# Performance work log

Hardware: AMD Instinct MI355X
Metric: run time of the kernel (lower is better)

The kernel has to match this reference:

```python
import jax, jax.numpy as jnp
import numpy as np

D_MODEL = 1024
N_HEADS = 16
HEAD_DIM = D_MODEL // N_HEADS
BATCH = 2
SEQ = 2048


def setup_inputs() -> dict:
    key = jax.random.key(0)
    ks = jax.random.split(key, 9)
    s = 1.0 / np.sqrt(D_MODEL)
    inp = {
        "x": jax.random.normal(ks[0], (BATCH, SEQ, D_MODEL), dtype=jnp.float32),
        "Wq": jax.random.uniform(ks[1], (D_MODEL, D_MODEL), jnp.float32, -s, s),
        "bq": jax.random.uniform(ks[2], (D_MODEL,), jnp.float32, -s, s),
        "Wk": jax.random.uniform(ks[3], (D_MODEL, D_MODEL), jnp.float32, -s, s),
        "bk": jax.random.uniform(ks[4], (D_MODEL,), jnp.float32, -s, s),
        "Wv": jax.random.uniform(ks[5], (D_MODEL, D_MODEL), jnp.float32, -s, s),
        "bv": jax.random.uniform(ks[6], (D_MODEL,), jnp.float32, -s, s),
        "Wo": jax.random.uniform(ks[7], (D_MODEL, D_MODEL), jnp.float32, -s, s),
        "bo": jax.random.uniform(ks[8], (D_MODEL,), jnp.float32, -s, s),
    }
    return inp


def reference(x, Wq, bq, Wk, bk, Wv, bv, Wo, bo):
    B, S, _ = x.shape
    # projections -> [B, H, S, Dh]
    def proj(W, b):
        y = jnp.einsum('bsd,df->bsf', x, W) + b
        return y.reshape(B, S, N_HEADS, HEAD_DIM).transpose(0, 2, 1, 3)
    q = proj(Wq, bq)
    k = proj(Wk, bk)
    v = proj(Wv, bv)
    scores = jnp.einsum('bhqd,bhkd->bhqk', q, k) / jnp.sqrt(jnp.float32(HEAD_DIM))
    mask = jnp.tril(jnp.ones((S, S), dtype=bool))  # [S, S] causal mask
    scores = jnp.where(mask, scores, -jnp.inf)
    weights = jax.nn.softmax(scores, axis=-1)
    h = jnp.einsum('bhqk,bhkd->bhqd', weights, v)
    h = h.transpose(0, 2, 1, 3).reshape(B, S, N_HEADS * HEAD_DIM)
    return jnp.einsum('bsd,df->bsf', h, Wo) + bo
```

## Files before the change

kernel.cpp:

```cpp
#include <hip/hip_runtime.h>
#include <hip/hip_bf16.h>
#include <cmath>

#define D_MODEL 1024
#define NHEADS 16
#define HDIM 64
#define BATCH 2
#define SEQ 2048
#define MROWS (BATCH*SEQ)
#define KDIM 1024

typedef unsigned short ushort_t;
typedef unsigned int uint32;
typedef __attribute__((ext_vector_type(8))) short short8;
typedef __attribute__((ext_vector_type(4))) float floatx4;

#define QSCALE 0.1803368801111204f
#define EXP2F(x) __builtin_amdgcn_exp2f(x)

__device__ __forceinline__ ushort_t f2bf(float x) {
    union { float f; uint32 u; } v; v.f = x;
    uint32 r = v.u + 0x7FFFu + ((v.u >> 16) & 1u);
    return (ushort_t)(r >> 16);
}

__device__ __forceinline__ uint32 pkbf(float a, float b) {
    union { __hip_bfloat162 h2; uint32 u; } v;
    v.h2 = __float22bfloat162_rn(make_float2(a, b));
    return v.u;
}

__device__ __forceinline__ void glds16(const void* g, void* l) {
    __builtin_amdgcn_global_load_lds(
        (const __attribute__((address_space(1))) void*)g,
        (__attribute__((address_space(3))) void*)l, 16, 0, 0);
}

__global__ __launch_bounds__(256)
void cvt_all(const float* __restrict__ x, const float* __restrict__ W0,
             const float* __restrict__ W1, const float* __restrict__ W2,
             const float* __restrict__ W3, ushort_t* __restrict__ xb,
             ushort_t* __restrict__ WtQKV, ushort_t* __restrict__ WtO)
{
    const int z = blockIdx.z;
    if (z == 4) {
        size_t idx = ((size_t)blockIdx.y * 32 + blockIdx.x) * 256 + threadIdx.x;
        #pragma unroll
        for (int l = 0; l < 4; ++l) {
            size_t i = ((size_t)l * 262144 + idx) * 4;
            float4 v = *(const float4*)(x + i);
            uint2 o;
            o.x = pkbf(v.x, v.y);
            o.y = pkbf(v.z, v.w);
            *(uint2*)(xb + i) = o;
        }
        return;
    }
    __shared__ float tl[32][33];
    const float* W = (z == 0) ? W0 : (z == 1) ? W1 : (z == 2) ? W2 : W3;
    ushort_t* out = (z < 3) ? (WtQKV + (size_t)z * D_MODEL * KDIM) : WtO;
    const int k0 = blockIdx.x * 32, n0 = blockIdx.y * 32;
    const int tx = threadIdx.x & 31, ty = threadIdx.x >> 5;
    #pragma unroll
    for (int i = 0; i < 4; ++i)
        tl[ty + i * 8][tx] = W[(size_t)(k0 + ty + i * 8) * D_MODEL + n0 + tx];
    __syncthreads();
    #pragma unroll
    for (int i = 0; i < 4; ++i)
        out[(size_t)(n0 + ty + i * 8) * KDIM + k0 + tx] = f2bf(tl[tx][ty + i * 8]);
}

__global__ __launch_bounds__(128, 2)
void gemm_qkv(const ushort_t* __restrict__ A, const ushort_t* __restrict__ Bt,
              const float* __restrict__ b0, const float* __restrict__ b1,
              const float* __restrict__ b2, ushort_t* __restrict__ Qb,
              ushort_t* __restrict__ Kb, ushort_t* __restrict__ Vb)
{
    __shared__ ushort_t As[128 * 64];
    __shared__ ushort_t Bs[128 * 64];

    const int tid = threadIdx.x;
    const int w = tid >> 6, lane = tid & 63;
    const int quad = lane >> 4, col = lane & 15;
    const int m0 = blockIdx.y * 128, n0 = blockIdx.x * 128;

    floatx4 zero = {0.f, 0.f, 0.f, 0.f};
    floatx4 acc[4][8];
    #pragma unroll
    for (int i = 0; i < 4; ++i)
        #pragma unroll
        for (int j = 0; j < 8; ++j) acc[i][j] = zero;

    #pragma unroll 1
    for (int k0 = 0; k0 < KDIM; k0 += 64) {
        #pragma unroll
        for (int i = 0; i < 8; ++i) {
            int c = i * 128 + tid;
            int row = c >> 3;
            int kc = (c & 7) ^ (row & 7);
            glds16(A  + (size_t)(m0 + row) * KDIM + k0 + kc * 8, As + (i * 128 + w * 64) * 8);
            glds16(Bt + (size_t)(n0 + row) * KDIM + k0 + kc * 8, Bs + (i * 128 + w * 64) * 8);
        }
        __syncthreads();
        #pragma unroll
        for (int ks = 0; ks < 2; ++ks) {
            short8 af[4], bfr[8];
            const int kc = ks * 4 + quad;
            #pragma unroll
            for (int mt = 0; mt < 4; ++mt) {
                int r = w * 64 + mt * 16 + col;
                af[mt] = *(const short8*)(As + ((size_t)r * 8 + (kc ^ (r & 7))) * 8);
            }
            #pragma unroll
            for (int nt = 0; nt < 8; ++nt) {
                int r = nt * 16 + col;
                bfr[nt] = *(const short8*)(Bs + ((size_t)r * 8 + (kc ^ (r & 7))) * 8);
            }
            #pragma unroll
            for (int mt = 0; mt < 4; ++mt)
                #pragma unroll
                for (int nt = 0; nt < 8; ++nt)
                    acc[mt][nt] = __builtin_amdgcn_mfma_f32_16x16x32_bf16(
                        af[mt], bfr[nt], acc[mt][nt], 0, 0, 0);
        }
        __syncthreads();
    }

    const int which = n0 >> 10;
    const float* bp = (which == 0) ? b0 : (which == 1) ? b1 : b2;
    if (which < 2) {
        ushort_t* outp = (which == 0) ? Qb : Kb;
        const float scl = (which == 0) ? QSCALE : 1.0f;
        #pragma unroll
        for (int mt = 0; mt < 4; ++mt)
            #pragma unroll
            for (int nt = 0; nt < 8; ++nt) {
                int nn = (n0 + nt * 16 + col) & 1023;
                float bb = bp[nn];
                int h = nn >> 6, d = nn & 63;
                #pragma unroll
                for (int r = 0; r < 4; ++r) {
                    int m = m0 + w * 64 + mt * 16 + quad * 4 + r;
                    int b = m >> 11, s = m & 2047;
                    outp[((size_t)(b * NHEADS + h) * SEQ + s) * HDIM + d] =
                        f2bf((acc[mt][nt][r] + bb) * scl);
                }
            }
    } else {
        #pragma unroll
        for (int mt = 0; mt < 4; ++mt)
            #pragma unroll
            for (int nt = 0; nt < 8; ++nt) {
                int nn = (n0 + nt * 16 + col) & 1023;
                float bb = bp[nn];
                int h = nn >> 6, d = nn & 63;
                int mb = m0 + w * 64 + mt * 16 + quad * 4;
                int b = mb >> 11, s = mb & 2047;
                uint2 pw;
                pw.x = pkbf(acc[mt][nt][0] + bb, acc[mt][nt][1] + bb);
                pw.y = pkbf(acc[mt][nt][2] + bb, acc[mt][nt][3] + bb);
                *(uint2*)(Vb + ((size_t)(b * NHEADS + h) * HDIM + d) * SEQ + s) = pw;
            }
    }
}

template<int BN>
__global__ __launch_bounds__(256)
void gemm_mfma(const ushort_t* __restrict__ A, const ushort_t* __restrict__ Bt,
               const float* __restrict__ b0, float* __restrict__ Cf)
{
    constexpr int NT = BN / 32;
    constexpr int BC = BN / 32;
    __shared__ ushort_t As[128 * 64];
    __shared__ ushort_t Bs[BN * 64];

    const int tid = threadIdx.x;
    const int w = tid >> 6, lane = tid & 63;
    const int quad = lane >> 4, col = lane & 15;
    const int m0 = blockIdx.y * 128, n0 = blockIdx.x * BN;
    const int mbase = (w & 1) * 64, nbase = (w >> 1) * (BN / 2);

    floatx4 zero = {0.f, 0.f, 0.f, 0.f};
    floatx4 acc[4][NT];
    #pragma unroll
    for (int i = 0; i < 4; ++i)
        #pragma unroll
        for (int j = 0; j < NT; ++j) acc[i][j] = zero;

    #pragma unroll 1
    for (int k0 = 0; k0 < KDIM; k0 += 64) {
        #pragma unroll
        for (int i = 0; i < 4; ++i) {
            int c = (w * 4 + i) * 64 + lane;
            int row = c >> 3;
            int kc = (c & 7) ^ (row & 7);
            glds16(A + (size_t)(m0 + row) * KDIM + k0 + kc * 8, As + (w * 4 + i) * 512);
        }
        #pragma unroll
        for (int i = 0; i < BC; ++i) {
            int c = (w * BC + i) * 64 + lane;
            int row = c >> 3;
            int kc = (c & 7) ^ (row & 7);
            glds16(Bt + (size_t)(n0 + row) * KDIM + k0 + kc * 8, Bs + (w * BC + i) * 512);
        }
        __syncthreads();
        #pragma unroll
        for (int ks = 0; ks < 2; ++ks) {
            short8 af[4], bfr[NT];
            const int kc = ks * 4 + quad;
            #pragma unroll
            for (int mt = 0; mt < 4; ++mt) {
                int r = mbase + mt * 16 + col;
                af[mt] = *(const short8*)(As + ((size_t)r * 8 + (kc ^ (r & 7))) * 8);
            }
            #pragma unroll
            for (int nt = 0; nt < NT; ++nt) {
                int r = nbase + nt * 16 + col;
                bfr[nt] = *(const short8*)(Bs + ((size_t)r * 8 + (kc ^ (r & 7))) * 8);
            }
            #pragma unroll
            for (int mt = 0; mt < 4; ++mt)
                #pragma unroll
                for (int nt = 0; nt < NT; ++nt)
                    acc[mt][nt] = __builtin_amdgcn_mfma_f32_16x16x32_bf16(
                        af[mt], bfr[nt], acc[mt][nt], 0, 0, 0);
        }
        __syncthreads();
    }

    #pragma unroll
    for (int mt = 0; mt < 4; ++mt)
        #pragma unroll
        for (int nt = 0; nt < NT; ++nt) {
            int n = n0 + nbase + nt * 16 + col;
            float bb = b0[n];
            #pragma unroll
            for (int r = 0; r < 4; ++r) {
                int m = m0 + mbase + mt * 16 + quad * 4 + r;
                Cf[(size_t)m * D_MODEL + n] = acc[mt][nt][r] + bb;
            }
        }
}

__global__ __launch_bounds__(256)
void attn_mfma(const ushort_t* __restrict__ Q, const ushort_t* __restrict__ K,
               const ushort_t* __restrict__ Vt, ushort_t* __restrict__ H)
{
    __shared__ ushort_t Qs[64 * 64];
    __shared__ ushort_t Ks[64 * 64];
    __shared__ ushort_t Vs[64 * 64];
    ushort_t* Ps = Qs;

    const int tid = threadIdx.x;
    const int w = tid >> 6, lane = tid & 63;
    const int quad = lane >> 4, col = lane & 15;
    const int blk = blockIdx.x;
    const int bh = (blk & 7) * 4 + ((blk >> 3) & 3);
    const int pair = blk >> 5;
    const size_t base = (size_t)bh * SEQ * HDIM;
    const ushort_t* Kb = K + base;
    const ushort_t* Vb = Vt + base;
    const int b = bh >> 4, h = bh & 15;

    const int c0 = (w * 2 + 0) * 64 + lane;
    const int c1 = (w * 2 + 1) * 64 + lane;
    const int r0 = c0 >> 3, o0 = ((c0 & 7) ^ (r0 & 7)) * 8;
    const int r1 = c1 >> 3, o1 = ((c1 & 7) ^ (r1 & 7)) * 8;

    const int qloc = w * 16 + col;
    const int rq = qloc;
    const floatx4 zero = {0.f, 0.f, 0.f, 0.f};

    #pragma unroll 1
    for (int pi = 0; pi < 2; ++pi) {
        const int qt = pi ? pair : 31 - pair;
        const int q0 = qt * 64;

        __syncthreads();
        #pragma unroll
        for (int i = 0; i < 2; ++i) {
            int c = (w * 2 + i) * 64 + lane;
            int row = c >> 3, kc = (c & 7) ^ (row & 7);
            glds16(Q + base + (size_t)(q0 + row) * HDIM + kc * 8, Qs + (w * 2 + i) * 512);
        }
        __syncthreads();
        short8 bq[2];
        #pragma unroll
        for (int ks = 0; ks < 2; ++ks) {
            int kc = ks * 4 + quad;
            bq[ks] = *(const short8*)(Qs + ((size_t)rq * 8 + (kc ^ (rq & 7))) * 8);
        }

        uint4 kr0 = *(const uint4*)(Kb + (size_t)r0 * HDIM + o0);
        uint4 kr1 = *(const uint4*)(Kb + (size_t)r1 * HDIM + o1);
        uint4 vr0 = *(const uint4*)(Vb + (size_t)r0 * SEQ + o0);
        uint4 vr1 = *(const uint4*)(Vb + (size_t)r1 * SEQ + o1);

        floatx4 o[4];
        #pragma unroll
        for (int j = 0; j < 4; ++j) o[j] = zero;
        float lreg = 0.f;

        const int nt = qt + 1;
        #pragma unroll 1
        for (int t = 0; t < nt; ++t) {
            __syncthreads();
            *(uint4*)(Ks + (size_t)c0 * 8) = kr0;
            *(uint4*)(Ks + (size_t)c1 * 8) = kr1;
            *(uint4*)(Vs + (size_t)c0 * 8) = vr0;
            *(uint4*)(Vs + (size_t)c1 * 8) = vr1;
            __syncthreads();
            if (t < nt - 1) {
                const int k0n = (t + 1) * 64;
                kr0 = *(const uint4*)(Kb + (size_t)(k0n + r0) * HDIM + o0);
                kr1 = *(const uint4*)(Kb + (size_t)(k0n + r1) * HDIM + o1);
                vr0 = *(const uint4*)(Vb + (size_t)r0 * SEQ + k0n + o0);
                vr1 = *(const uint4*)(Vb + (size_t)r1 * SEQ + k0n + o1);
            }

            floatx4 sc[4];
            #pragma unroll
            for (int j = 0; j < 4; ++j) sc[j] = zero;
            #pragma unroll
            for (int ks = 0; ks < 2; ++ks) {
                const int kc = ks * 4 + quad;
                #pragma unroll
                for (int j = 0; j < 4; ++j) {
                    int rk = j * 16 + col;
                    short8 ak = *(const short8*)(Ks + ((size_t)rk * 8 + (kc ^ (rk & 7))) * 8);
                    sc[j] = __builtin_amdgcn_mfma_f32_16x16x32_bf16(ak, bq[ks], sc[j], 0, 0, 0);
                }
            }

            if (t == nt - 1) {
                #pragma unroll
                for (int j = 0; j < 4; ++j)
                    #pragma unroll
                    for (int r = 0; r < 4; ++r)
                        if (j * 16 + quad * 4 + r > qloc) sc[j][r] = -INFINITY;
            }

            float ls = 0.f;
            #pragma unroll
            for (int j = 0; j < 4; ++j) {
                float p0 = EXP2F(sc[j][0]);
                float p1 = EXP2F(sc[j][1]);
                float p2 = EXP2F(sc[j][2]);
                float p3 = EXP2F(sc[j][3]);
                ls += (p0 + p1) + (p2 + p3);
                uint2 pw;
                pw.x = pkbf(p0, p1);
                pw.y = pkbf(p2, p3);
                int c = 2 * j + (quad >> 1);
                *(uint2*)(Ps + ((size_t)rq * 8 + (c ^ (rq & 7))) * 8 + (quad & 1) * 4) = pw;
            }
            lreg += ls;

            #pragma unroll
            for (int ks = 0; ks < 2; ++ks) {
                const int kc = ks * 4 + quad;
                short8 bp = *(const short8*)(Ps + ((size_t)rq * 8 + (kc ^ (rq & 7))) * 8);
                #pragma unroll
                for (int j = 0; j < 4; ++j) {
                    int rv = j * 16 + col;
                    short8 av = *(const short8*)(Vs + ((size_t)rv * 8 + (kc ^ (rv & 7))) * 8);
                    o[j] = __builtin_amdgcn_mfma_f32_16x16x32_bf16(av, bp, o[j], 0, 0, 0);
                }
            }
        }

        lreg += __shfl_xor(lreg, 16);
        lreg += __shfl_xor(lreg, 32);

        const float linv = 1.f / lreg;
        const size_t rowb = ((size_t)(b * SEQ + q0 + qloc)) * D_MODEL + h * HDIM;
        #pragma unroll
        for (int j = 0; j < 4; ++j) {
            uint2 pw;
            pw.x = pkbf(o[j][0] * linv, o[j][1] * linv);
            pw.y = pkbf(o[j][2] * linv, o[j][3] * linv);
            *(uint2*)(H + rowb + j * 16 + quad * 4) = pw;
        }
    }
}

extern "C" void kernel_launch(void* const* d_in, const int* in_sizes, int n_in,
                              void* d_out, int out_size, void* d_ws, size_t ws_size,
                              hipStream_t stream)
{
    (void)in_sizes; (void)n_in; (void)out_size; (void)ws_size;
    const float* x  = (const float*)d_in[0];
    const float* Wq = (const float*)d_in[1];
    const float* bq = (const float*)d_in[2];
    const float* Wk = (const float*)d_in[3];
    const float* bk = (const float*)d_in[4];
    const float* Wv = (const float*)d_in[5];
    const float* bv = (const float*)d_in[6];
    const float* Wo = (const float*)d_in[7];
    const float* bo = (const float*)d_in[8];

    const size_t E = (size_t)MROWS * D_MODEL;
    ushort_t* xb    = (ushort_t*)d_ws;
    ushort_t* WtQKV = xb + E;
    ushort_t* WtO   = WtQKV + 3 * (size_t)D_MODEL * KDIM;
    ushort_t* Qb    = WtO + (size_t)D_MODEL * KDIM;
    ushort_t* Kb    = Qb + E;
    ushort_t* Vb    = Kb + E;
    ushort_t* Hb    = Vb + E;

    cvt_all<<<dim3(32, 32, 5), 256, 0, stream>>>(x, Wq, Wk, Wv, Wo, xb, WtQKV, WtO);
    gemm_qkv<<<dim3(24, 32), 128, 0, stream>>>(xb, WtQKV, bq, bk, bv, Qb, Kb, Vb);
    attn_mfma<<<dim3(512), 256, 0, stream>>>(Qb, Kb, Vb, Hb);
    gemm_mfma<64><<<dim3(16, 32), 256, 0, stream>>>(Hb, WtO, bo, (float*)d_out);
}
```

Before: 181.5 us.

## Double-buffer K/V in attention with async global-to-LDS loads; reshape output GEMM

The attention kernel now loads K and V tiles straight from global memory into LDS through two buffers, instead of staging them in registers and storing them. This cuts the barriers per key tile from two to one and overlaps the next tile's load with the current tile's MFMA work. In exchange it doubles the K/V LDS footprint, which may lower occupancy. The output projection GEMM is also changed to 128-thread blocks of two waves, each computing a 64x64 tile, with a two-blocks-per-CU launch bound.

```diff
diff --git a/kernel.cpp b/kernel.cpp
--- a/kernel.cpp
+++ b/kernel.cpp
@@ -164,64 +164,60 @@
     }
 }
 
-template<int BN>
-__global__ __launch_bounds__(256)
-void gemm_mfma(const ushort_t* __restrict__ A, const ushort_t* __restrict__ Bt,
-               const float* __restrict__ b0, float* __restrict__ Cf)
+__global__ __launch_bounds__(128, 2)
+void gemm_o(const ushort_t* __restrict__ A, const ushort_t* __restrict__ Bt,
+            const float* __restrict__ b0, float* __restrict__ Cf)
 {
-    constexpr int NT = BN / 32;
-    constexpr int BC = BN / 32;
     __shared__ ushort_t As[128 * 64];
-    __shared__ ushort_t Bs[BN * 64];
+    __shared__ ushort_t Bs[64 * 64];
 
     const int tid = threadIdx.x;
     const int w = tid >> 6, lane = tid & 63;
     const int quad = lane >> 4, col = lane & 15;
-    const int m0 = blockIdx.y * 128, n0 = blockIdx.x * BN;
-    const int mbase = (w & 1) * 64, nbase = (w >> 1) * (BN / 2);
+    const int m0 = blockIdx.y * 128, n0 = blockIdx.x * 64;
 
     floatx4 zero = {0.f, 0.f, 0.f, 0.f};
-    floatx4 acc[4][NT];
+    floatx4 acc[4][4];
     #pragma unroll
     for (int i = 0; i < 4; ++i)
         #pragma unroll
-        for (int j = 0; j < NT; ++j) acc[i][j] = zero;
+        for (int j = 0; j < 4; ++j) acc[i][j] = zero;
 
     #pragma unroll 1
     for (int k0 = 0; k0 < KDIM; k0 += 64) {
         #pragma unroll
-        for (int i = 0; i < 4; ++i) {
-            int c = (w * 4 + i) * 64 + lane;
+        for (int i = 0; i < 8; ++i) {
+            int c = i * 128 + tid;
             int row = c >> 3;
             int kc = (c & 7) ^ (row & 7);
-            glds16(A + (size_t)(m0 + row) * KDIM + k0 + kc * 8, As + (w * 4 + i) * 512);
-        }
-        #pragma unroll
-        for (int i = 0; i < BC; ++i) {
-            int c = (w * BC + i) * 64 + lane;
+            glds16(A + (size_t)(m0 + row) * KDIM + k0 + kc * 8, As + (i * 128 + w * 64) * 8);
+        }
+        #pragma unroll
+        for (int i = 0; i < 4; ++i) {
+            int c = i * 128 + tid;
             int row = c >> 3;
             int kc = (c & 7) ^ (row & 7);
-            glds16(Bt + (size_t)(n0 + row) * KDIM + k0 + kc * 8, Bs + (w * BC + i) * 512);
+            glds16(Bt + (size_t)(n0 + row) * KDIM + k0 + kc * 8, Bs + (i * 128 + w * 64) * 8);
         }
         __syncthreads();
         #pragma unroll
         for (int ks = 0; ks < 2; ++ks) {
-            short8 af[4], bfr[NT];
+            short8 af[4], bfr[4];
             const int kc = ks * 4 + quad;
             #pragma unroll
             for (int mt = 0; mt < 4; ++mt) {
-                int r = mbase + mt * 16 + col;
+                int r = w * 64 + mt * 16 + col;
                 af[mt] = *(const short8*)(As + ((size_t)r * 8 + (kc ^ (r & 7))) * 8);
             }
             #pragma unroll
-            for (int nt = 0; nt < NT; ++nt) {
-                int r = nbase + nt * 16 + col;
+            for (int nt = 0; nt < 4; ++nt) {
+                int r = nt * 16 + col;
                 bfr[nt] = *(const short8*)(Bs + ((size_t)r * 8 + (kc ^ (r & 7))) * 8);
             }
             #pragma unroll
             for (int mt = 0; mt < 4; ++mt)
                 #pragma unroll
-                for (int nt = 0; nt < NT; ++nt)
+                for (int nt = 0; nt < 4; ++nt)
                     acc[mt][nt] = __builtin_amdgcn_mfma_f32_16x16x32_bf16(
                         af[mt], bfr[nt], acc[mt][nt], 0, 0, 0);
         }
@@ -231,12 +227,12 @@
     #pragma unroll
     for (int mt = 0; mt < 4; ++mt)
         #pragma unroll
-        for (int nt = 0; nt < NT; ++nt) {
-            int n = n0 + nbase + nt * 16 + col;
+        for (int nt = 0; nt < 4; ++nt) {
+            int n = n0 + nt * 16 + col;
             float bb = b0[n];
             #pragma unroll
             for (int r = 0; r < 4; ++r) {
-                int m = m0 + mbase + mt * 16 + quad * 4 + r;
+                int m = m0 + w * 64 + mt * 16 + quad * 4 + r;
                 Cf[(size_t)m * D_MODEL + n] = acc[mt][nt][r] + bb;
             }
         }
@@ -247,8 +243,8 @@
                const ushort_t* __restrict__ Vt, ushort_t* __restrict__ H)
 {
     __shared__ ushort_t Qs[64 * 64];
-    __shared__ ushort_t Ks[64 * 64];
-    __shared__ ushort_t Vs[64 * 64];
+    __shared__ ushort_t Ks[2][64 * 64];
+    __shared__ ushort_t Vs[2][64 * 64];
     ushort_t* Ps = Qs;
 
     const int tid = threadIdx.x;
@@ -275,6 +271,7 @@
     for (int pi = 0; pi < 2; ++pi) {
         const int qt = pi ? pair : 31 - pair;
         const int q0 = qt * 64;
+        const int nt = qt + 1;
 
         __syncthreads();
         #pragma unroll
@@ -283,7 +280,12 @@
             int row = c >> 3, kc = (c & 7) ^ (row & 7);
             glds16(Q + base + (size_t)(q0 + row) * HDIM + kc * 8, Qs + (w * 2 + i) * 512);
         }
-        __syncthreads();
+        glds16(Kb + (size_t)r0 * HDIM + o0, Ks[0] + (w * 2 + 0) * 512);
+        glds16(Kb + (size_t)r1 * HDIM + o1, Ks[0] + (w * 2 + 1) * 512);
+        glds16(Vb + (size_t)r0 * SEQ + o0,  Vs[0] + (w * 2 + 0) * 512);
+        glds16(Vb + (size_t)r1 * SEQ + o1,  Vs[0] + (w * 2 + 1) * 512);
+        __syncthreads();
+
         short8 bq[2];
         #pragma unroll
         for (int ks = 0; ks < 2; ++ks) {
@@ -291,31 +293,23 @@
             bq[ks] = *(const short8*)(Qs + ((size_t)rq * 8 + (kc ^ (rq & 7))) * 8);
         }
 
-        uint4 kr0 = *(const uint4*)(Kb + (size_t)r0 * HDIM + o0);
-        uint4 kr1 = *(const uint4*)(Kb + (size_t)r1 * HDIM + o1);
-        uint4 vr0 = *(const uint4*)(Vb + (size_t)r0 * SEQ + o0);
-        uint4 vr1 = *(const uint4*)(Vb + (size_t)r1 * SEQ + o1);
-
         floatx4 o[4];
         #pragma unroll
         for (int j = 0; j < 4; ++j) o[j] = zero;
         float lreg = 0.f;
 
-        const int nt = qt + 1;
         #pragma unroll 1
         for (int t = 0; t < nt; ++t) {
-            __syncthreads();
-            *(uint4*)(Ks + (size_t)c0 * 8) = kr0;
-            *(uint4*)(Ks + (size_t)c1 * 8) = kr1;
-            *(uint4*)(Vs + (size_t)c0 * 8) = vr0;
-            *(uint4*)(Vs + (size_t)c1 * 8) = vr1;
-            __syncthreads();
-            if (t < nt - 1) {
+            const ushort_t* Kcur = Ks[t & 1];
+            const ushort_t* Vcur = Vs[t & 1];
+            if (t + 1 < nt) {
                 const int k0n = (t + 1) * 64;
-                kr0 = *(const uint4*)(Kb + (size_t)(k0n + r0) * HDIM + o0);
-                kr1 = *(const uint4*)(Kb + (size_t)(k0n + r1) * HDIM + o1);
-                vr0 = *(const uint4*)(Vb + (size_t)r0 * SEQ + k0n + o0);
-                vr1 = *(const uint4*)(Vb + (size_t)r1 * SEQ + k0n + o1);
+                ushort_t* Kn = Ks[(t + 1) & 1];
+                ushort_t* Vn = Vs[(t + 1) & 1];
+                glds16(Kb + (size_t)(k0n + r0) * HDIM + o0, Kn + (w * 2 + 0) * 512);
+                glds16(Kb + (size_t)(k0n + r1) * HDIM + o1, Kn + (w * 2 + 1) * 512);
+                glds16(Vb + (size_t)r0 * SEQ + k0n + o0,    Vn + (w * 2 + 0) * 512);
+                glds16(Vb + (size_t)r1 * SEQ + k0n + o1,    Vn + (w * 2 + 1) * 512);
             }
 
             floatx4 sc[4];
@@ -327,7 +321,7 @@
                 #pragma unroll
                 for (int j = 0; j < 4; ++j) {
                     int rk = j * 16 + col;
-                    short8 ak = *(const short8*)(Ks + ((size_t)rk * 8 + (kc ^ (rk & 7))) * 8);
+                    short8 ak = *(const short8*)(Kcur + ((size_t)rk * 8 + (kc ^ (rk & 7))) * 8);
                     sc[j] = __builtin_amdgcn_mfma_f32_16x16x32_bf16(ak, bq[ks], sc[j], 0, 0, 0);
                 }
             }
@@ -363,10 +357,12 @@
                 #pragma unroll
                 for (int j = 0; j < 4; ++j) {
                     int rv = j * 16 + col;
-                    short8 av = *(const short8*)(Vs + ((size_t)rv * 8 + (kc ^ (rv & 7))) * 8);
+                    short8 av = *(const short8*)(Vcur + ((size_t)rv * 8 + (kc ^ (rv & 7))) * 8);
                     o[j] = __builtin_amdgcn_mfma_f32_16x16x32_bf16(av, bp, o[j], 0, 0, 0);
                 }
             }
+
+            __syncthreads();
         }
 
         lreg += __shfl_xor(lreg, 16);
@@ -411,5 +407,5 @@
     cvt_all<<<dim3(32, 32, 5), 256, 0, stream>>>(x, Wq, Wk, Wv, Wo, xb, WtQKV, WtO);
     gemm_qkv<<<dim3(24, 32), 128, 0, stream>>>(xb, WtQKV, bq, bk, bv, Qb, Kb, Vb);
     attn_mfma<<<dim3(512), 256, 0, stream>>>(Qb, Kb, Vb, Hb);
-    gemm_mfma<64><<<dim3(16, 32), 256, 0, stream>>>(Hb, WtO, bo, (float*)d_out);
-}
+    gemm_o<<<dim3(16, 32), 128, 0, stream>>>(Hb, WtO, bo, (float*)d_out);
+}
```

Measured after the change: 177.4 us. 2.3% less time.
